# Performance work log

Measured on AMD Instinct MI355X. Metric: run time of the kernel, lower is better.

Reference implementation:

```python
import jax, jax.numpy as jnp
import numpy as np

B, T, C, H = 2, 2048, 1024, 16
HS = C // H                      # head_size = 64
LAYER_IDX = 2
LAMBDA_INIT = 0.8 - 0.6 * float(np.exp(-0.3 * (LAYER_IDX - 1)))
EPS = 1e-12


def setup_inputs() -> dict:
    key = jax.random.key(0)
    ks = jax.random.split(key, 22)
    std = 0.02
    w = lambda k, shape: (jax.random.normal(k, shape, jnp.float32) * std)
    inp = {
        'q': jax.random.normal(ks[0], (B, T, C), jnp.float32),
        'k': jax.random.normal(ks[1], (B, T, C), jnp.float32),
        'v': jax.random.normal(ks[2], (B, T, C), jnp.float32),
        'mask': jax.random.randint(ks[3], (B, T), 0, 2).astype(jnp.int32),
        # projection weights stored as (in, out) so y = x @ W + b
        'Wq1': w(ks[4], (C, C)), 'bq1': jnp.zeros((C,), jnp.float32),
        'Wq2': w(ks[5], (C, C)), 'bq2': jnp.zeros((C,), jnp.float32),
        'Wk1': w(ks[6], (C, C)), 'bk1': jnp.zeros((C,), jnp.float32),
        'Wk2': w(ks[7], (C, C)), 'bk2': jnp.zeros((C,), jnp.float32),
        'Wv':  w(ks[8], (C, 2 * C)), 'bv': jnp.zeros((2 * C,), jnp.float32),
        'Wc':  w(ks[9], (2 * C, C)), 'bc': jnp.zeros((C,), jnp.float32),
        'ln_w': jnp.ones((2 * HS,), jnp.float32),
        'ln_b': jnp.zeros((2 * HS,), jnp.float32),
        'lq1': jax.random.normal(ks[10], (H, HS), jnp.float32) * 0.1,
        'lk1': jax.random.normal(ks[11], (H, HS), jnp.float32) * 0.1,
        'lq2': jax.random.normal(ks[12], (H, HS), jnp.float32) * 0.1,
        'lk2': jax.random.normal(ks[13], (H, HS), jnp.float32) * 0.1,
    }
    return inp


def reference(q, k, v, mask, Wq1, bq1, Wq2, bq2, Wk1, bk1, Wk2, bk2,
              Wv, bv, Wc, bc, ln_w, ln_b, lq1, lk1, lq2, lk2):
    def heads(x, d):  # [B,T,H*d] -> [B,H,T,d]
        return x.reshape(B, T, H, d).transpose(0, 2, 1, 3)

    q1 = heads(q @ Wq1 + bq1, HS)
    q2 = heads(q @ Wq2 + bq2, HS)
    k1 = heads(k @ Wk1 + bk1, HS)
    k2 = heads(k @ Wk2 + bk2, HS)
    vv = heads(v @ Wv + bv, 2 * HS)          # [B,H,T,2*HS]

    scale = 1.0 / np.sqrt(HS)
    att1 = jnp.einsum('bhqd,bhkd->bhqk', q1, k1) * scale
    att2 = jnp.einsum('bhqd,bhkd->bhqk', q2, k2) * scale

    m = (mask == 0)[:, None, :, None]         # [B,1,Tq,1] -> masks query rows
    att1 = jnp.where(m, -1e9, att1)
    att2 = jnp.where(m, -1e9, att2)
    att1 = jax.nn.softmax(att1, axis=-1)
    att2 = jax.nn.softmax(att2, axis=-1)

    lam1 = jnp.exp(jnp.sum(lq1 * lk1, axis=-1))   # [H]
    lam2 = jnp.exp(jnp.sum(lq2 * lk2, axis=-1))
    lam = (lam1 - lam2 + LAMBDA_INIT)[None, :, None, None]
    att = att1 - lam * att2                       # differential attention

    y = jnp.einsum('bhqk,bhkd->bhqd', att, vv)    # [B,H,T,2*HS]

    # per-head TF-style LayerNorm over 2*HS, then (1 - lambda_init) scale
    u = y.mean(-1, keepdims=True)
    s = ((y - u) ** 2).mean(-1, keepdims=True)
    y = ln_w * ((y - u) / jnp.sqrt(s + EPS)) + ln_b
    y = y * (1.0 - LAMBDA_INIT)

    y = y.transpose(0, 2, 1, 3).reshape(B, T, 2 * C)
    return y @ Wc + bc
```

## Files before the change

### kernel.cpp

```cpp
#include <hip/hip_runtime.h>
#include <hip/hip_bf16.h>
#include <stdint.h>


#define T_SEQ 2048

typedef unsigned short u16;
typedef __attribute__((ext_vector_type(8))) short short8;
typedef __attribute__((ext_vector_type(4))) float f32x4;
typedef __attribute__((ext_vector_type(16))) float f32x16;

#define LAMBDA_INIT 0.35550906759096926f
#define ONE_MINUS_LI 0.6444909324090307f
#define SM_SCALE 0.125f

__device__ __forceinline__ u16 f2bf(float f) {
  uint32_t u = __float_as_uint(f);
  return (u16)((u + 0x7FFFu + ((u >> 16) & 1u)) >> 16);
}
__device__ __forceinline__ float b2f(u16 u) {
  return __uint_as_float(((uint32_t)u) << 16);
}
__device__ __forceinline__ short8 ld8(const u16* p) {
  return *reinterpret_cast<const short8*>(p);
}
__device__ __forceinline__ void st8(u16* p, short8 v) {
  *reinterpret_cast<short8*>(p) = v;
}
__device__ __forceinline__ f32x4 mfma16(short8 a, short8 b, f32x4 c) {
  return __builtin_amdgcn_mfma_f32_16x16x32_bf16(a, b, c, 0, 0, 0);
}
__device__ __forceinline__ f32x16 mfma32(short8 a, short8 b, f32x16 c) {
  return __builtin_amdgcn_mfma_f32_32x32x16_bf16(a, b, c, 0, 0, 0);
}
__device__ __forceinline__ uint32_t cvtpk(float lo, float hi_) {
  uint32_t r;
  asm("v_cvt_pk_bf16_f32 %0, %1, %2" : "=v"(r) : "v"(lo), "v"(hi_));
  return r;
}

__global__ __launch_bounds__(256) void cvt_bf16(const float* __restrict__ in,
                                                u16* __restrict__ out, int n) {
  int i = (blockIdx.x * 256 + threadIdx.x) * 4;
  if (i >= n) return;
  float4 f = *reinterpret_cast<const float4*>(in + i);
  union { u16 u[4]; uint2 v; } pk;
  pk.u[0] = f2bf(f.x); pk.u[1] = f2bf(f.y); pk.u[2] = f2bf(f.z); pk.u[3] = f2bf(f.w);
  *reinterpret_cast<uint2*>(out + i) = pk.v;
}

__global__ __launch_bounds__(256) void tcvt(const float* __restrict__ W,
                                            u16* __restrict__ WT,
                                            int K, int N, int outRowOff) {
  __shared__ float tile[32][33];
  int n0 = blockIdx.x * 32, k0 = blockIdx.y * 32;
  int tx = threadIdx.x & 31, ty = threadIdx.x >> 5;
#pragma unroll
  for (int p = 0; p < 4; ++p)
    tile[ty + 8 * p][tx] = W[(size_t)(k0 + ty + 8 * p) * N + n0 + tx];
  __syncthreads();
#pragma unroll
  for (int p = 0; p < 4; ++p)
    WT[(size_t)(outRowOff + n0 + ty + 8 * p) * K + k0 + tx] = f2bf(tile[tx][ty + 8 * p]);
}

__global__ __launch_bounds__(256) void bias_concat(const float* __restrict__ b1,
                                                   const float* __restrict__ b2,
                                                   float* __restrict__ out) {
  int i = blockIdx.x * 256 + threadIdx.x;
  out[i] = (i < 1024) ? b1[i] : b2[i - 1024];
}

#define BM 128
#define BN 128
#define BK 32

template <int EPI>
__global__ __launch_bounds__(256) void gemm_bt(const u16* __restrict__ A,
                                               const u16* __restrict__ BT,
                                               const float* __restrict__ bias,
                                               void* __restrict__ Cv,
                                               int M, int N, int K) {
  __shared__ __align__(16) u16 As[BM * BK];
  __shared__ __align__(16) u16 Bs[BN * BK];
  int t = threadIdx.x;
  int w = t >> 6, l = t & 63;
  int g = l >> 4, c16 = l & 15;
  int wr = w >> 1, wc = w & 1;
  size_t gm = (size_t)blockIdx.y * BM, gn = (size_t)blockIdx.x * BN;

  f32x4 acc[4][4] = {};

  int srow = w * 16 + (l >> 2);
  int scol = (l & 3) * 8;
  const u16* Ag = A + (gm + srow) * (size_t)K + scol;
  const u16* Bg = BT + (gn + srow) * (size_t)K + scol;

  for (int kt = 0; kt < K; kt += BK) {
    __syncthreads();
#pragma unroll
    for (int ca = 0; ca < 2; ++ca) {
      __builtin_amdgcn_global_load_lds(
          (const __attribute__((address_space(1))) void*)(Ag + (size_t)(ca * 64) * K + kt),
          (__attribute__((address_space(3))) void*)&As[(ca * 64 + w * 16) * BK], 16, 0, 0);
      __builtin_amdgcn_global_load_lds(
          (const __attribute__((address_space(1))) void*)(Bg + (size_t)(ca * 64) * K + kt),
          (__attribute__((address_space(3))) void*)&Bs[(ca * 64 + w * 16) * BK], 16, 0, 0);
    }
    __syncthreads();
    short8 af[4], bf[4];
#pragma unroll
    for (int m = 0; m < 4; ++m)
      af[m] = *reinterpret_cast<const short8*>(&As[(wr * 64 + m * 16 + c16) * BK + g * 8]);
#pragma unroll
    for (int n = 0; n < 4; ++n)
      bf[n] = *reinterpret_cast<const short8*>(&Bs[(wc * 64 + n * 16 + c16) * BK + g * 8]);
#pragma unroll
    for (int m = 0; m < 4; ++m)
#pragma unroll
      for (int n = 0; n < 4; ++n)
        acc[m][n] = mfma16(af[m], bf[n], acc[m][n]);
  }

#pragma unroll
  for (int m = 0; m < 4; ++m)
#pragma unroll
    for (int n = 0; n < 4; ++n) {
      int row0 = (int)gm + wr * 64 + m * 16 + g * 4;
      int col = (int)gn + wc * 64 + n * 16 + c16;
      float bz = bias[col];
      if (EPI == 0) {
        u16* C = (u16*)Cv;
#pragma unroll
        for (int r = 0; r < 4; ++r)
          C[(size_t)(row0 + r) * N + col] = f2bf(acc[m][n][r] + bz);
      } else if (EPI == 1) {
        u16* C = (u16*)Cv;
        int bb = row0 >> 11, tt = row0 & 2047;
        union { u16 u[4]; uint2 v; } pk;
#pragma unroll
        for (int r = 0; r < 4; ++r) pk.u[r] = f2bf(acc[m][n][r] + bz);
        *reinterpret_cast<uint2*>(&C[((size_t)(bb * 2048 + col)) * 2048 + tt]) = pk.v;
      } else {
        float* C = (float*)Cv;
#pragma unroll
        for (int r = 0; r < 4; ++r)
          C[(size_t)(row0 + r) * N + col] = acc[m][n][r] + bz;
      }
    }
}

#define KROW 72
#define VROW 40
#define YROW 72
__global__ __launch_bounds__(256, 3) void diffattn(
    const u16* __restrict__ q1q2, const u16* __restrict__ k1k2,
    const u16* __restrict__ vvT, const int* __restrict__ mask,
    const float* __restrict__ lq1, const float* __restrict__ lk1,
    const float* __restrict__ lq2, const float* __restrict__ lk2,
    const float* __restrict__ lnw, const float* __restrict__ lnb,
    u16* __restrict__ yout) {
  __shared__ __align__(16) u16 smem[9728];
  u16* Ksm = smem;
  u16* Vsm = smem + 4608;
  u16* Ysm = smem;

  int tid = threadIdx.x;
  int w = tid >> 6, l = tid & 63;
  int q = l & 31, hi = l >> 5;
  int pair = w >> 1, stream = w & 1;
  int bh = blockIdx.y, b = bh >> 4, h = bh & 15;
  int qr0 = blockIdx.x * 64 + pair * 32;

  float lm1 = lq1[h * 64 + l] * lk1[h * 64 + l];
  float lm2 = lq2[h * 64 + l] * lk2[h * 64 + l];
#pragma unroll
  for (int o = 32; o; o >>= 1) {
    lm1 += __shfl_xor(lm1, o);
    lm2 += __shfl_xor(lm2, o);
  }
  float lam = __expf(lm1) - __expf(lm2) + LAMBDA_INIT;

  int soff = stream * 1024;
  const u16* qrow = q1q2 + (size_t)(b * T_SEQ + qr0 + q) * 2048 + h * 64 + soff + hi * 8;
  short8 qf[4];
#pragma unroll
  for (int c = 0; c < 4; ++c) qf[c] = ld8(qrow + c * 16);

  float scale = (mask[b * T_SEQ + qr0 + q] == 0) ? 0.f : SM_SCALE;

  float M = -INFINITY, L = 0.f;
  f32x16 acc[4] = {};

  int ku = tid * 2;
  int krow = ku >> 3, kslot = ku & 7;
  int kstream = krow >> 5, kkey = krow & 31;
  const u16* srcK = k1k2 + (size_t)(b * T_SEQ + kkey) * 2048 + h * 64 + kstream * 1024 + kslot * 8;
  u16* dstK = &Ksm[(kstream * 32 + kkey) * KROW + kslot * 8];
  int vd = tid >> 1, vslot = (tid & 1) * 2;
  const u16* srcV = vvT + ((size_t)(b * 16 + h) * 128 + vd) * 2048 + vslot * 8;
  u16* dstV = &Vsm[vd * VROW + vslot * 8];

  short8 kr0 = ld8(srcK), kr1 = ld8(srcK + 8);
  short8 vr0 = ld8(srcV), vr1 = ld8(srcV + 8);

  for (int kt = 0; kt < T_SEQ; kt += 32) {
    __syncthreads();
    st8(dstK, kr0); st8(dstK + 8, kr1);
    st8(dstV, vr0); st8(dstV + 8, vr1);
    __syncthreads();
    if (kt + 32 < T_SEQ) {
      const u16* nk = srcK + (size_t)(kt + 32) * 2048;
      kr0 = ld8(nk); kr1 = ld8(nk + 8);
      const u16* nv = srcV + (kt + 32);
      vr0 = ld8(nv); vr1 = ld8(nv + 8);
    }

    const u16* kbase = &Ksm[(stream * 32 + q) * KROW + hi * 8];
    short8 kf[4];
#pragma unroll
    for (int c = 0; c < 4; ++c) kf[c] = ld8(kbase + c * 16);

    f32x16 s = {};
#pragma unroll
    for (int c = 0; c < 4; ++c) s = mfma32(kf[c], qf[c], s);

    float x[16];
#pragma unroll
    for (int r = 0; r < 16; ++r) x[r] = s[r] * scale;

    float t8[8], t4[4];
#pragma unroll
    for (int i = 0; i < 8; ++i) t8[i] = fmaxf(x[i], x[i + 8]);
#pragma unroll
    for (int i = 0; i < 4; ++i) t4[i] = fmaxf(t8[i], t8[i + 4]);
    float tm = fmaxf(fmaxf(t4[0], t4[1]), fmaxf(t4[2], t4[3]));
    tm = fmaxf(tm, __shfl_xor(tm, 32));

    if (!__all(tm - M <= 8.f)) {
      float Mn = fmaxf(M, tm);
      float a = __expf(M - Mn);
      L *= a;
#pragma unroll
      for (int d = 0; d < 4; ++d) acc[d] *= a;
      M = Mn;
    }

    float p[16];
#pragma unroll
    for (int r = 0; r < 16; ++r) p[r] = __expf(x[r] - M);
    float s8[8], s4[4];
#pragma unroll
    for (int i = 0; i < 8; ++i) s8[i] = p[i] + p[i + 8];
#pragma unroll
    for (int i = 0; i < 4; ++i) s4[i] = s8[i] + s8[i + 4];
    float ps = (s4[0] + s4[1]) + (s4[2] + s4[3]);
    ps += __shfl_xor(ps, 32);
    L += ps;

    uint32_t a1 = cvtpk(p[0], p[1]), a2 = cvtpk(p[2], p[3]);
    uint32_t b1 = cvtpk(p[4], p[5]), b2 = cvtpk(p[6], p[7]);
    uint32_t c1 = cvtpk(p[8], p[9]), c2 = cvtpk(p[10], p[11]);
    uint32_t d1 = cvtpk(p[12], p[13]), d2 = cvtpk(p[14], p[15]);
    uint32_t sa1 = (uint32_t)__shfl_xor((int)a1, 32), sa2 = (uint32_t)__shfl_xor((int)a2, 32);
    uint32_t sb1 = (uint32_t)__shfl_xor((int)b1, 32), sb2 = (uint32_t)__shfl_xor((int)b2, 32);
    uint32_t sc1 = (uint32_t)__shfl_xor((int)c1, 32), sc2 = (uint32_t)__shfl_xor((int)c2, 32);
    uint32_t sd1 = (uint32_t)__shfl_xor((int)d1, 32), sd2 = (uint32_t)__shfl_xor((int)d2, 32);
    union { uint32_t u[4]; short8 s8v; } pu0, pu1;
    pu0.u[0] = hi ? sb1 : a1;  pu0.u[1] = hi ? sb2 : a2;
    pu0.u[2] = hi ? b1 : sa1;  pu0.u[3] = hi ? b2 : sa2;
    pu1.u[0] = hi ? sd1 : c1;  pu1.u[1] = hi ? sd2 : c2;
    pu1.u[2] = hi ? d1 : sc1;  pu1.u[3] = hi ? d2 : sc2;
    short8 pf0 = pu0.s8v, pf1 = pu1.s8v;

#pragma unroll
    for (int d = 0; d < 4; ++d) {
      const u16* vb0 = &Vsm[(d * 32 + q) * VROW + hi * 8];
      short8 vf0 = ld8(vb0);
      short8 vf1 = ld8(vb0 + 16);
      acc[d] = mfma32(vf0, pf0, acc[d]);
      acc[d] = mfma32(vf1, pf1, acc[d]);
    }
  }

  float inv = 1.f / L;
  __syncthreads();
  if (stream == 1) {
    u16* yrow = &Ysm[(pair * 64 + l) * YROW];
#pragma unroll
    for (int d = 0; d < 4; ++d) {
      union { uint32_t u[8]; short8 v[2]; } pk;
#pragma unroll
      for (int i = 0; i < 8; ++i)
        pk.u[i] = cvtpk(acc[d][2 * i] * inv, acc[d][2 * i + 1] * inv);
      st8(yrow + d * 16, pk.v[0]);
      st8(yrow + d * 16 + 8, pk.v[1]);
    }
  }
  __syncthreads();
  if (stream == 0) {
    const u16* yrow = &Ysm[(pair * 64 + l) * YROW];
    float y[4][16];
#pragma unroll
    for (int d = 0; d < 4; ++d) {
      short8 y2a = ld8(yrow + d * 16);
      short8 y2b = ld8(yrow + d * 16 + 8);
#pragma unroll
      for (int i = 0; i < 8; ++i) {
        y[d][i] = acc[d][i] * inv - lam * b2f((u16)y2a[i]);
        y[d][8 + i] = acc[d][8 + i] * inv - lam * b2f((u16)y2b[i]);
      }
    }
    float sm = 0.f;
#pragma unroll
    for (int d = 0; d < 4; ++d)
#pragma unroll
      for (int r = 0; r < 16; ++r) sm += y[d][r];
    sm += __shfl_xor(sm, 32);
    float u = sm * (1.f / 128.f);
    float var = 0.f;
#pragma unroll
    for (int d = 0; d < 4; ++d)
#pragma unroll
      for (int r = 0; r < 16; ++r) { float dd = y[d][r] - u; var += dd * dd; }
    var += __shfl_xor(var, 32);
    float rstd = rsqrtf(var * (1.f / 128.f) + 1e-12f);

    size_t orow = (size_t)(b * T_SEQ + qr0 + q) * 2048 + h * 128;
#pragma unroll
    for (int d = 0; d < 4; ++d)
#pragma unroll
      for (int rr = 0; rr < 4; ++rr) {
        int base = d * 32 + 8 * rr + 4 * hi;
        union { u16 u[4]; uint2 v; } o;
#pragma unroll
        for (int i = 0; i < 4; ++i) {
          float yv = (lnw[base + i] * ((y[d][rr * 4 + i] - u) * rstd) + lnb[base + i]) *
                     ONE_MINUS_LI;
          o.u[i] = f2bf(yv);
        }
        *reinterpret_cast<uint2*>(&yout[orow + base]) = o.v;
      }
  }
}

extern "C" void kernel_launch(void* const* d_in, const int* in_sizes, int n_in,
                              void* d_out, int out_size, void* d_ws, size_t ws_size,
                              hipStream_t stream) {
  (void)in_sizes; (void)n_in; (void)out_size; (void)ws_size;
  const float* q   = (const float*)d_in[0];
  const float* k   = (const float*)d_in[1];
  const float* v   = (const float*)d_in[2];
  const int* maskp = (const int*)d_in[3];
  const float* Wq1 = (const float*)d_in[4];
  const float* bq1 = (const float*)d_in[5];
  const float* Wq2 = (const float*)d_in[6];
  const float* bq2 = (const float*)d_in[7];
  const float* Wk1 = (const float*)d_in[8];
  const float* bk1 = (const float*)d_in[9];
  const float* Wk2 = (const float*)d_in[10];
  const float* bk2 = (const float*)d_in[11];
  const float* Wv  = (const float*)d_in[12];
  const float* bv  = (const float*)d_in[13];
  const float* Wc  = (const float*)d_in[14];
  const float* bc  = (const float*)d_in[15];
  const float* lnw = (const float*)d_in[16];
  const float* lnb = (const float*)d_in[17];
  const float* lq1 = (const float*)d_in[18];
  const float* lk1 = (const float*)d_in[19];
  const float* lq2 = (const float*)d_in[20];
  const float* lk2 = (const float*)d_in[21];

  char* ws = (char*)d_ws;
  u16* qb     = (u16*)(ws + 0);
  u16* kb     = (u16*)(ws + 8388608);
  u16* vb     = (u16*)(ws + 16777216);
  u16* Wq12T  = (u16*)(ws + 25165824);
  u16* Wk12T  = (u16*)(ws + 29360128);
  u16* WvT    = (u16*)(ws + 33554432);
  u16* WcT    = (u16*)(ws + 37748736);
  float* biasq = (float*)(ws + 41943040);
  float* biask = (float*)(ws + 41951232);
  u16* q1q2   = (u16*)(ws + 41959424);
  u16* k1k2   = (u16*)(ws + 58736640);
  u16* vvT    = (u16*)(ws + 75513856);
  u16* yb     = (u16*)(ws + 0);

  const int NELEM = 2 * T_SEQ * 1024;

  cvt_bf16<<<4096, 256, 0, stream>>>(q, qb, NELEM);
  cvt_bf16<<<4096, 256, 0, stream>>>(k, kb, NELEM);
  cvt_bf16<<<4096, 256, 0, stream>>>(v, vb, NELEM);

  tcvt<<<dim3(32, 32), 256, 0, stream>>>(Wq1, Wq12T, 1024, 1024, 0);
  tcvt<<<dim3(32, 32), 256, 0, stream>>>(Wq2, Wq12T, 1024, 1024, 1024);
  tcvt<<<dim3(32, 32), 256, 0, stream>>>(Wk1, Wk12T, 1024, 1024, 0);
  tcvt<<<dim3(32, 32), 256, 0, stream>>>(Wk2, Wk12T, 1024, 1024, 1024);
  tcvt<<<dim3(64, 32), 256, 0, stream>>>(Wv, WvT, 1024, 2048, 0);
  tcvt<<<dim3(32, 64), 256, 0, stream>>>(Wc, WcT, 2048, 1024, 0);

  bias_concat<<<8, 256, 0, stream>>>(bq1, bq2, biasq);
  bias_concat<<<8, 256, 0, stream>>>(bk1, bk2, biask);

  gemm_bt<0><<<dim3(16, 32), 256, 0, stream>>>(qb, Wq12T, biasq, q1q2, 4096, 2048, 1024);
  gemm_bt<0><<<dim3(16, 32), 256, 0, stream>>>(kb, Wk12T, biask, k1k2, 4096, 2048, 1024);
  gemm_bt<1><<<dim3(16, 32), 256, 0, stream>>>(vb, WvT, bv, vvT, 4096, 2048, 1024);

  diffattn<<<dim3(32, 32), 256, 0, stream>>>(q1q2, k1k2, vvT, maskp,
                                             lq1, lk1, lq2, lk2, lnw, lnb, yb);

  gemm_bt<2><<<dim3(8, 32), 256, 0, stream>>>(yb, WcT, bc, d_out, 4096, 1024, 2048);
}
```

Measured before the change: 328.8 us.

## Double-buffer K/V in attention, use exp2 softmax, raise GEMM BK to 64

The attention kernel now double-buffers the K/V shared-memory tiles. The next tile is stored after the MFMA work, so each iteration needs one barrier instead of two. Softmax switches to exp2 with log2e folded into the scale, the lazy-rescale threshold is adjusted to match, and occupancy bounds go from 3 to 4 blocks. The GEMM K-tile doubles to 64, halving loop iterations and barriers, at the cost of more LDS per block; the doubled attention LDS could also limit occupancy.

```diff
diff --git a/kernel.cpp b/kernel.cpp
--- a/kernel.cpp
+++ b/kernel.cpp
@@ -13,6 +13,7 @@
 #define LAMBDA_INIT 0.35550906759096926f
 #define ONE_MINUS_LI 0.6444909324090307f
 #define SM_SCALE 0.125f
+#define LOG2E 1.44269504f
 
 __device__ __forceinline__ u16 f2bf(float f) {
   uint32_t u = __float_as_uint(f);
@@ -73,7 +74,7 @@
 
 #define BM 128
 #define BN 128
-#define BK 32
+#define BK 64
 
 template <int EPI>
 __global__ __launch_bounds__(256) void gemm_bt(const u16* __restrict__ A,
@@ -91,35 +92,40 @@
 
   f32x4 acc[4][4] = {};
 
-  int srow = w * 16 + (l >> 2);
-  int scol = (l & 3) * 8;
-  const u16* Ag = A + (gm + srow) * (size_t)K + scol;
-  const u16* Bg = BT + (gn + srow) * (size_t)K + scol;
+  int srow = l >> 3;
+  int scol = (l & 7) * 8;
+  const u16* Ag = A + (gm + w * 32 + srow) * (size_t)K + scol;
+  const u16* Bg = BT + (gn + w * 32 + srow) * (size_t)K + scol;
 
   for (int kt = 0; kt < K; kt += BK) {
     __syncthreads();
 #pragma unroll
-    for (int ca = 0; ca < 2; ++ca) {
+    for (int c = 0; c < 4; ++c) {
       __builtin_amdgcn_global_load_lds(
-          (const __attribute__((address_space(1))) void*)(Ag + (size_t)(ca * 64) * K + kt),
-          (__attribute__((address_space(3))) void*)&As[(ca * 64 + w * 16) * BK], 16, 0, 0);
+          (const __attribute__((address_space(1))) void*)(Ag + (size_t)(c * 8) * K + kt),
+          (__attribute__((address_space(3))) void*)&As[(w * 32 + c * 8) * BK], 16, 0, 0);
       __builtin_amdgcn_global_load_lds(
-          (const __attribute__((address_space(1))) void*)(Bg + (size_t)(ca * 64) * K + kt),
-          (__attribute__((address_space(3))) void*)&Bs[(ca * 64 + w * 16) * BK], 16, 0, 0);
+          (const __attribute__((address_space(1))) void*)(Bg + (size_t)(c * 8) * K + kt),
+          (__attribute__((address_space(3))) void*)&Bs[(w * 32 + c * 8) * BK], 16, 0, 0);
     }
     __syncthreads();
-    short8 af[4], bf[4];
-#pragma unroll
-    for (int m = 0; m < 4; ++m)
-      af[m] = *reinterpret_cast<const short8*>(&As[(wr * 64 + m * 16 + c16) * BK + g * 8]);
-#pragma unroll
-    for (int n = 0; n < 4; ++n)
-      bf[n] = *reinterpret_cast<const short8*>(&Bs[(wc * 64 + n * 16 + c16) * BK + g * 8]);
-#pragma unroll
-    for (int m = 0; m < 4; ++m)
+#pragma unroll
+    for (int kk = 0; kk < 2; ++kk) {
+      short8 af[4], bf[4];
+#pragma unroll
+      for (int m = 0; m < 4; ++m)
+        af[m] = *reinterpret_cast<const short8*>(
+            &As[(wr * 64 + m * 16 + c16) * BK + kk * 32 + g * 8]);
 #pragma unroll
       for (int n = 0; n < 4; ++n)
-        acc[m][n] = mfma16(af[m], bf[n], acc[m][n]);
+        bf[n] = *reinterpret_cast<const short8*>(
+            &Bs[(wc * 64 + n * 16 + c16) * BK + kk * 32 + g * 8]);
+#pragma unroll
+      for (int m = 0; m < 4; ++m)
+#pragma unroll
+        for (int n = 0; n < 4; ++n)
+          acc[m][n] = mfma16(af[m], bf[n], acc[m][n]);
+    }
   }
 
 #pragma unroll
@@ -153,17 +159,14 @@
 #define KROW 72
 #define VROW 40
 #define YROW 72
-__global__ __launch_bounds__(256, 3) void diffattn(
+__global__ __launch_bounds__(256, 4) void diffattn(
     const u16* __restrict__ q1q2, const u16* __restrict__ k1k2,
     const u16* __restrict__ vvT, const int* __restrict__ mask,
     const float* __restrict__ lq1, const float* __restrict__ lk1,
     const float* __restrict__ lq2, const float* __restrict__ lk2,
     const float* __restrict__ lnw, const float* __restrict__ lnb,
     u16* __restrict__ yout) {
-  __shared__ __align__(16) u16 smem[9728];
-  u16* Ksm = smem;
-  u16* Vsm = smem + 4608;
-  u16* Ysm = smem;
+  __shared__ __align__(16) u16 smem[2][9728];
 
   int tid = threadIdx.x;
   int w = tid >> 6, l = tid & 63;
@@ -187,7 +190,7 @@
 #pragma unroll
   for (int c = 0; c < 4; ++c) qf[c] = ld8(qrow + c * 16);
 
-  float scale = (mask[b * T_SEQ + qr0 + q] == 0) ? 0.f : SM_SCALE;
+  float scale = (mask[b * T_SEQ + qr0 + q] == 0) ? 0.f : (SM_SCALE * LOG2E);
 
   float M = -INFINITY, L = 0.f;
   f32x16 acc[4] = {};
@@ -196,26 +199,33 @@
   int krow = ku >> 3, kslot = ku & 7;
   int kstream = krow >> 5, kkey = krow & 31;
   const u16* srcK = k1k2 + (size_t)(b * T_SEQ + kkey) * 2048 + h * 64 + kstream * 1024 + kslot * 8;
-  u16* dstK = &Ksm[(kstream * 32 + kkey) * KROW + kslot * 8];
+  int dK = (kstream * 32 + kkey) * KROW + kslot * 8;
   int vd = tid >> 1, vslot = (tid & 1) * 2;
   const u16* srcV = vvT + ((size_t)(b * 16 + h) * 128 + vd) * 2048 + vslot * 8;
-  u16* dstV = &Vsm[vd * VROW + vslot * 8];
-
-  short8 kr0 = ld8(srcK), kr1 = ld8(srcK + 8);
-  short8 vr0 = ld8(srcV), vr1 = ld8(srcV + 8);
-
+  int dV = 4608 + vd * VROW + vslot * 8;
+
+  {
+    short8 k0 = ld8(srcK), k1v = ld8(srcK + 8);
+    short8 v0 = ld8(srcV), v1 = ld8(srcV + 8);
+    st8(&smem[0][dK], k0); st8(&smem[0][dK + 8], k1v);
+    st8(&smem[0][dV], v0); st8(&smem[0][dV + 8], v1);
+  }
+  __syncthreads();
+
+  short8 kr0, kr1, vr0, vr1;
   for (int kt = 0; kt < T_SEQ; kt += 32) {
-    __syncthreads();
-    st8(dstK, kr0); st8(dstK + 8, kr1);
-    st8(dstV, vr0); st8(dstV + 8, vr1);
-    __syncthreads();
-    if (kt + 32 < T_SEQ) {
+    int cur = (kt >> 5) & 1;
+    bool more = (kt + 32 < T_SEQ);
+    if (more) {
       const u16* nk = srcK + (size_t)(kt + 32) * 2048;
       kr0 = ld8(nk); kr1 = ld8(nk + 8);
       const u16* nv = srcV + (kt + 32);
       vr0 = ld8(nv); vr1 = ld8(nv + 8);
     }
 
+    const u16* Ksm = &smem[cur][0];
+    const u16* Vsm = &smem[cur][4608];
+
     const u16* kbase = &Ksm[(stream * 32 + q) * KROW + hi * 8];
     short8 kf[4];
 #pragma unroll
@@ -237,9 +247,9 @@
     float tm = fmaxf(fmaxf(t4[0], t4[1]), fmaxf(t4[2], t4[3]));
     tm = fmaxf(tm, __shfl_xor(tm, 32));
 
-    if (!__all(tm - M <= 8.f)) {
+    if (!__all(tm - M <= 11.5f)) {
       float Mn = fmaxf(M, tm);
-      float a = __expf(M - Mn);
+      float a = exp2f(M - Mn);
       L *= a;
 #pragma unroll
       for (int d = 0; d < 4; ++d) acc[d] *= a;
@@ -248,7 +258,7 @@
 
     float p[16];
 #pragma unroll
-    for (int r = 0; r < 16; ++r) p[r] = __expf(x[r] - M);
+    for (int r = 0; r < 16; ++r) p[r] = exp2f(x[r] - M);
     float s8[8], s4[4];
 #pragma unroll
     for (int i = 0; i < 8; ++i) s8[i] = p[i] + p[i + 8];
@@ -281,10 +291,17 @@
       acc[d] = mfma32(vf0, pf0, acc[d]);
       acc[d] = mfma32(vf1, pf1, acc[d]);
     }
+
+    if (more) {
+      u16* nb = &smem[cur ^ 1][0];
+      st8(&nb[dK], kr0); st8(&nb[dK + 8], kr1);
+      st8(&nb[dV], vr0); st8(&nb[dV + 8], vr1);
+    }
+    __syncthreads();
   }
 
   float inv = 1.f / L;
-  __syncthreads();
+  u16* Ysm = &smem[0][0];
   if (stream == 1) {
     u16* yrow = &Ysm[(pair * 64 + l) * YROW];
 #pragma unroll
```

Measured after the change: 352.7 us. 7.3% more time.
